# Optimization experiments

Hardware: AMD Instinct MI355X
Metric: run time of the kernel (lower is better)

## Reference

```python
import jax, jax.numpy as jnp
import numpy as np

N = 40000        # nodes (shared across categories)
E = 600000       # edges per category graph
H = 2            # heads
C = 64           # hidden (out_channels per head)
IN_DIMS = [128, 128, 64]
FUSED = H * C * len(IN_DIMS)  # 384


def setup_inputs() -> dict:
    key = jax.random.key(0)
    ks = iter(jax.random.split(key, 64))
    d = {}
    for i, din in enumerate(IN_DIMS):
        d[f"x{i}"] = jax.random.normal(next(ks), (N, din), jnp.float32)
        d[f"ei{i}"] = jax.random.randint(next(ks), (2, E), 0, N)
        d[f"W{i}"] = jax.random.normal(next(ks), (din, H * C), jnp.float32) / np.sqrt(din)
        d[f"att_s{i}"] = jax.random.normal(next(ks), (H, C), jnp.float32) * 0.1
        d[f"att_d{i}"] = jax.random.normal(next(ks), (H, C), jnp.float32) * 0.1
        d[f"bias{i}"] = jnp.zeros((H * C,), jnp.float32)
    d["Wc1"] = jax.random.normal(next(ks), (FUSED, 128), jnp.float32) / np.sqrt(FUSED)
    d["bc1"] = jnp.zeros((128,), jnp.float32)
    d["Wc2"] = jax.random.normal(next(ks), (128, 1), jnp.float32) / np.sqrt(128.0)
    d["bc2"] = jnp.zeros((1,), jnp.float32)
    return d


def gat_conv(x, edge_index, W, att_s, att_d, bias):
    """PyG GATConv (concat=True, add_self_loops=True, eval mode)."""
    n = x.shape[0]
    xw = (x @ W).reshape(n, H, C)                       # [N,H,C]
    a_src = jnp.einsum('nhc,hc->nh', xw, att_s)         # [N,H]
    a_dst = jnp.einsum('nhc,hc->nh', xw, att_d)         # [N,H]
    loop = jnp.arange(n)
    src = jnp.concatenate([edge_index[0], loop])        # [E+N]
    dst = jnp.concatenate([edge_index[1], loop])
    e = jax.nn.leaky_relu(a_src[src] + a_dst[dst], 0.2)  # [E+N,H]
    # segment softmax over incoming edges per destination node
    m = jax.lax.stop_gradient(jax.ops.segment_max(e, dst, num_segments=n))
    ex = jnp.exp(e - m[dst])
    s = jax.ops.segment_sum(ex, dst, num_segments=n)
    alpha = ex / s[dst]                                  # [E+N,H]
    out = jax.ops.segment_sum(xw[src] * alpha[..., None], dst, num_segments=n)
    return out.reshape(n, H * C) + bias


def reference(x0, ei0, W0, att_s0, att_d0, bias0,
              x1, ei1, W1, att_s1, att_d1, bias1,
              x2, ei2, W2, att_s2, att_d2, bias2,
              Wc1, bc1, Wc2, bc2):
    h0 = jax.nn.elu(gat_conv(x0, ei0, W0, att_s0, att_d0, bias0))
    h1 = jax.nn.elu(gat_conv(x1, ei1, W1, att_s1, att_d1, bias1))
    h2 = jax.nn.elu(gat_conv(x2, ei2, W2, att_s2, att_d2, bias2))
    Hcat = jnp.concatenate([h0, h1, h2], axis=-1)        # [N, FUSED]
    hid = jax.nn.relu(Hcat @ Wc1 + bc1)
    return hid @ Wc2 + bc2                               # [N, 1]
```

## Files before the change

### kernel.cpp

```cpp
#include <hip/hip_runtime.h>
#include <hip/hip_fp16.h>
#include <cstdint>
#include <cstddef>


__device__ __forceinline__ float lrelu02(float x) { return x > 0.f ? x : 0.2f * x; }
__device__ __forceinline__ float elu1(float x) { return x > 0.f ? x : (__expf(x) - 1.f); }

__device__ __forceinline__ unsigned bfrne(float x) {
  unsigned u = __float_as_uint(x);
  return (u + 0x7FFFu + ((u >> 16) & 1u)) >> 16;
}
__device__ __forceinline__ unsigned pack2bf(float lo, float hi) {
  return bfrne(lo) | (bfrne(hi) << 16);
}
__device__ __forceinline__ float bflo2f(unsigned u) { return __uint_as_float(u << 16); }
__device__ __forceinline__ float bfhi2f(unsigned u) { return __uint_as_float(u & 0xFFFF0000u); }

__device__ __forceinline__ unsigned pack2half(float lo, float hi) {
  __half2 h2 = __floats2half2_rn(lo, hi);
  return __builtin_bit_cast(unsigned, h2);
}
__device__ __forceinline__ float h2lo(unsigned u) {
  return __half2float(__low2half(__builtin_bit_cast(__half2, u)));
}
__device__ __forceinline__ float h2hi(unsigned u) {
  return __half2float(__high2half(__builtin_bit_cast(__half2, u)));
}

typedef __attribute__((ext_vector_type(8))) short short8;
typedef __attribute__((ext_vector_type(4))) float f32x4;

#define SLICES 8
#define CAPX 448
#define BCAP (SLICES * CAPX)

#define SBS 512
#define SEPT 16
#define STB (SBS * SEPT)
#define NBINS_PAD 1024

__global__ void zeroB(int* __restrict__ a, int n) {
  int i = blockIdx.x * blockDim.x + threadIdx.x;
  if (i < n) a[i] = 0;
}

__global__ void w_swz(const float* __restrict__ W,
                      unsigned short* __restrict__ wsw, int nt) {
  int idx = blockIdx.x * blockDim.x + threadIdx.x;
  if (idx >= nt * 8 * 64) return;
  int l = idx & 63;
  int n = (idx >> 6) & 7;
  int t = idx >> 9;
  int col = n * 16 + (l & 15);
  int kbase = t * 32 + (l >> 4) * 8;
  uint4 o;
  o.x = pack2bf(W[(kbase + 0) * 128 + col], W[(kbase + 1) * 128 + col]);
  o.y = pack2bf(W[(kbase + 2) * 128 + col], W[(kbase + 3) * 128 + col]);
  o.z = pack2bf(W[(kbase + 4) * 128 + col], W[(kbase + 5) * 128 + col]);
  o.w = pack2bf(W[(kbase + 6) * 128 + col], W[(kbase + 7) * 128 + col]);
  *(uint4*)(wsw + (size_t)idx * 8) = o;
}

__global__ __launch_bounds__(256) void gemm_att_mfma(
    const float* __restrict__ X, const unsigned short* __restrict__ wsw,
    const float* __restrict__ att_s, const float* __restrict__ att_d,
    unsigned short* __restrict__ XWH, float* __restrict__ a_src,
    float* __restrict__ a_dst, int M, int K) {
  const int tid = threadIdx.x;
  const int l = tid & 63;
  const int w = tid >> 6;
  const int lrow = l & 15;
  const int lk = (l >> 4) * 8;
  const int row0 = blockIdx.x * 64 + w * 16;
  int arow = row0 + lrow; if (arow >= M) arow = M - 1;
  const float* aptr = X + (size_t)arow * K + lk;
  const unsigned short* bptr = wsw + (size_t)l * 8;
  const int nt = K >> 5;

  f32x4 acc[8];
#pragma unroll
  for (int n = 0; n < 8; ++n) acc[n] = (f32x4){0.f, 0.f, 0.f, 0.f};

  for (int t = 0; t < nt; ++t) {
    float4 xa = *(const float4*)(aptr + t * 32);
    float4 xb = *(const float4*)(aptr + t * 32 + 4);
    uint4 av;
    av.x = pack2bf(xa.x, xa.y);
    av.y = pack2bf(xa.z, xa.w);
    av.z = pack2bf(xb.x, xb.y);
    av.w = pack2bf(xb.z, xb.w);
    short8 af = __builtin_bit_cast(short8, av);
#pragma unroll
    for (int n = 0; n < 8; ++n) {
      uint4 bv = *(const uint4*)(bptr + (size_t)(t * 8 + n) * 512);
      short8 bf = __builtin_bit_cast(short8, bv);
      acc[n] = __builtin_amdgcn_mfma_f32_16x16x32_bf16(af, bf, acc[n], 0, 0, 0);
    }
  }

  float as_[8], ad_[8];
#pragma unroll
  for (int n = 0; n < 8; ++n) {
    int col = n * 16 + lrow;
    as_[n] = att_s[col];
    ad_[n] = att_d[col];
  }
#pragma unroll
  for (int r = 0; r < 4; ++r) {
    int wrow = row0 + (l >> 4) * 4 + r;
    const bool ok = wrow < M;
    float ps0 = 0.f, ps1 = 0.f, pd0 = 0.f, pd1 = 0.f;
#pragma unroll
    for (int n = 0; n < 8; ++n) {
      float v = acc[n][r];
      if (ok) XWH[(size_t)wrow * 128 + n * 16 + lrow] = (unsigned short)bfrne(v);
      if (n < 4) { ps0 = fmaf(v, as_[n], ps0); pd0 = fmaf(v, ad_[n], pd0); }
      else       { ps1 = fmaf(v, as_[n], ps1); pd1 = fmaf(v, ad_[n], pd1); }
    }
#pragma unroll
    for (int off = 1; off < 16; off <<= 1) {
      ps0 += __shfl_xor(ps0, off); ps1 += __shfl_xor(ps1, off);
      pd0 += __shfl_xor(pd0, off); pd1 += __shfl_xor(pd1, off);
    }
    if (lrow == 0 && ok) {
      ((float2*)a_src)[wrow] = make_float2(ps0, ps1);
      ((float2*)a_dst)[wrow] = make_float2(pd0, pd1);
    }
  }
}

__global__ __launch_bounds__(512) void scatter_p(
    const int* __restrict__ ei0, const int* __restrict__ ei1,
    const int* __restrict__ ei2, int E0, int E1, int E2,
    int nbpc, int* __restrict__ bktCnt, int* __restrict__ bkt) {
  __shared__ int hist[NBINS_PAD];
  __shared__ int binStart[NBINS_PAD];
  __shared__ int binResv[NBINS_PAD];
  __shared__ int fillB[NBINS_PAD];
  __shared__ int scanBuf[SBS];
  __shared__ int stage[STB];
  __shared__ int gdst[STB];
  const int tid = threadIdx.x;
  const int slice = blockIdx.x & (SLICES - 1);
  const int nbins = 3 * nbpc;
  const int c1 = E0, c2 = E0 + E1, totE = c2 + E2;
  const int eb = blockIdx.x * STB;

  for (int b = tid; b < NBINS_PAD; b += SBS) hist[b] = 0;
  __syncthreads();

  int binv[SEPT], payv[SEPT];
#pragma unroll
  for (int k = 0; k < SEPT; ++k) {
    int g = eb + k * SBS + tid;
    int bn = -1, pay = 0;
    if (g < totE) {
      int s, d, cat;
      if (g < c1)      { s = ei0[g]; d = ei0[E0 + g]; cat = 0; }
      else if (g < c2) { int t = g - c1; s = ei1[t]; d = ei1[E1 + t]; cat = 1; }
      else             { int t = g - c2; s = ei2[t]; d = ei2[E2 + t]; cat = 2; }
      bn = cat * nbpc + (d >> 7);
      pay = ((d & 127) << 16) | s;
      atomicAdd(&hist[bn], 1);
    }
    binv[k] = bn; payv[k] = pay;
  }
  __syncthreads();

  const int a0 = hist[tid * 2], a1 = hist[tid * 2 + 1];
  scanBuf[tid] = a0 + a1;
  __syncthreads();
  for (int off = 1; off < SBS; off <<= 1) {
    int v = (tid >= off) ? scanBuf[tid - off] : 0;
    __syncthreads();
    scanBuf[tid] += v;
    __syncthreads();
  }
  const int total = scanBuf[SBS - 1];
  const int base = (tid > 0) ? scanBuf[tid - 1] : 0;
  binStart[tid * 2] = base;
  binStart[tid * 2 + 1] = base + a0;

  for (int b = tid; b < NBINS_PAD; b += SBS) {
    fillB[b] = 0;
    int c = hist[b];
    if (c > 0 && b < nbins)
      binResv[b] = atomicAdd(&bktCnt[(b * SLICES + slice) * 16], c);
  }
  __syncthreads();

#pragma unroll
  for (int k = 0; k < SEPT; ++k) {
    int bn = binv[k];
    if (bn >= 0) {
      int f = atomicAdd(&fillB[bn], 1);
      int p = binStart[bn] + f;
      int go = binResv[bn] + f;
      stage[p] = payv[k];
      gdst[p] = (go < CAPX) ? ((bn * SLICES + slice) * CAPX + go) : -1;
    }
  }
  __syncthreads();

  for (int i = tid; i < total; i += SBS) {
    int g = gdst[i];
    if (g >= 0) bkt[g] = stage[i];
  }
}

__global__ __launch_bounds__(256) void sortbkt(
    int* __restrict__ bkt, const int* __restrict__ bktCnt,
    int2* __restrict__ offcnt, int Nn, int nbpc) {
  __shared__ int cntA[128], scanA[128], fillA[128];
  __shared__ int esort[BCAP];
  const int tid = threadIdx.x;
  const int b = blockIdx.x;
  const int cat = b / nbpc, bl = b - cat * nbpc, dBase = bl << 7;
  if (tid < 128) {
    cntA[tid] = (dBase + tid < Nn) ? 1 : 0;
    fillA[tid] = 0;
  }
  __syncthreads();
  int ns[SLICES];
#pragma unroll
  for (int s = 0; s < SLICES; ++s)
    ns[s] = min(bktCnt[(b * SLICES + s) * 16], CAPX);
#pragma unroll
  for (int s = 0; s < SLICES; ++s) {
    const int* seg = bkt + (size_t)(b * SLICES + s) * CAPX;
    for (int i = tid; i < ns[s]; i += 256) atomicAdd(&cntA[seg[i] >> 16], 1);
  }
  __syncthreads();
  if (tid < 128) scanA[tid] = cntA[tid];
  __syncthreads();
  for (int off = 1; off < 128; off <<= 1) {
    int t = (tid < 128 && tid >= off) ? scanA[tid - off] : 0;
    __syncthreads();
    if (tid < 128) scanA[tid] += t;
    __syncthreads();
  }
#pragma unroll
  for (int s = 0; s < SLICES; ++s) {
    const int* seg = bkt + (size_t)(b * SLICES + s) * CAPX;
    for (int i = tid; i < ns[s]; i += 256) {
      int v = seg[i];
      int n = v >> 16;
      int p = scanA[n] - cntA[n] + atomicAdd(&fillA[n], 1);
      esort[p] = v & 0xFFFF;
    }
  }
  if (tid < 128 && dBase + tid < Nn) esort[scanA[tid] - 1] = dBase + tid;
  __syncthreads();
  const int tot = scanA[127];
  int* outp = bkt + (size_t)b * BCAP;
  for (int i = tid; i < tot; i += 256) outp[i] = esort[i];
  if (tid < 128 && dBase + tid < Nn)
    offcnt[(size_t)cat * Nn + dBase + tid] =
        make_int2(b * BCAP + scanA[tid] - cntA[tid], cntA[tid]);
}

__global__ __launch_bounds__(256) void aggregate(
    const unsigned short* __restrict__ xwh, const float* __restrict__ a_src,
    const float* __restrict__ a_dst, const int2* __restrict__ offcnt,
    const int* __restrict__ adjS, const float* __restrict__ bias,
    unsigned short* __restrict__ ahc, int Nn) {
  const int tid = threadIdx.x;
  const int lane = tid & 63;
  const int li = lane & 15;
  const int gb = lane & 48;
  const int wid = (int)((blockIdx.x * (size_t)blockDim.x + tid) >> 6);
  const int node = wid * 4 + (lane >> 4);
  const bool nok = node < Nn;
  const int cnode = nok ? node : Nn - 1;
  const int2 oc = offcnt[cnode];
  const int base = oc.x;
  const int cnt = oc.y;
  const float2 ad = ((const float2*)a_dst)[cnode];

  float m0 = -1e30f, s0 = 0.f, m1 = -1e30f, s1 = 0.f;
  int sv0 = 0; float ex0 = -1e30f, ey0 = -1e30f;
  for (int cb = 0; cb < cnt; cb += 16) {
    int sv = 0; float ex = -1e30f, ey = -1e30f;
    if (cb + li < cnt) {
      sv = adjS[base + cb + li];
      float2 as = ((const float2*)a_src)[sv];
      ex = lrelu02(as.x + ad.x);
      ey = lrelu02(as.y + ad.y);
      float nm0 = fmaxf(m0, ex);
      s0 = s0 * __expf(m0 - nm0) + __expf(ex - nm0); m0 = nm0;
      float nm1 = fmaxf(m1, ey);
      s1 = s1 * __expf(m1 - nm1) + __expf(ey - nm1); m1 = nm1;
    }
    if (cb == 0) { sv0 = sv; ex0 = ex; ey0 = ey; }
  }
#pragma unroll
  for (int off = 8; off; off >>= 1) {
    float om0 = __shfl_xor(m0, off), os0 = __shfl_xor(s0, off);
    float nm0 = fmaxf(m0, om0);
    s0 = s0 * __expf(m0 - nm0) + os0 * __expf(om0 - nm0); m0 = nm0;
    float om1 = __shfl_xor(m1, off), os1 = __shfl_xor(s1, off);
    float nm1 = fmaxf(m1, om1);
    s1 = s1 * __expf(m1 - nm1) + os1 * __expf(om1 - nm1); m1 = nm1;
  }
  const float inv0 = 1.f / s0, inv1 = 1.f / s1;

  int mc = cnt;
  mc = max(mc, __shfl_xor(mc, 16));
  mc = max(mc, __shfl_xor(mc, 32));

  const bool hlo = (li < 8);
  float acc[8];
#pragma unroll
  for (int c = 0; c < 8; ++c) acc[c] = 0.f;

  for (int cb = 0; cb < mc; cb += 16) {
    int sv; float ex, ey;
    if (cb == 0) { sv = sv0; ex = ex0; ey = ey0; }
    else {
      sv = 0; ex = -1e30f; ey = -1e30f;
      if (cb + li < cnt) {
        sv = adjS[base + cb + li];
        float2 as = ((const float2*)a_src)[sv];
        ex = lrelu02(as.x + ad.x);
        ey = lrelu02(as.y + ad.y);
      }
    }
    const float w0 = __expf(ex - m0) * inv0;
    const float w1 = __expf(ey - m1) * inv1;
    const unsigned wpk = pack2half(w0, w1);

    int cc = cnt - cb; cc = cc < 0 ? 0 : (cc > 16 ? 16 : cc);
    cc = max(cc, __shfl_xor(cc, 16));
    cc = max(cc, __shfl_xor(cc, 32));

    int k = 0;
    for (; k + 2 <= cc; k += 2) {
      int ska = __shfl(sv, gb + k);
      int skb = __shfl(sv, gb + k + 1);
      unsigned wka = __shfl(wpk, gb + k);
      unsigned wkb = __shfl(wpk, gb + k + 1);
      uint4 ua = *(const uint4*)(xwh + (size_t)ska * 128 + li * 8);
      uint4 ub = *(const uint4*)(xwh + (size_t)skb * 128 + li * 8);
      float wa = hlo ? h2lo(wka) : h2hi(wka);
      float wb = hlo ? h2lo(wkb) : h2hi(wkb);
      acc[0] = fmaf(wa, bflo2f(ua.x), acc[0]); acc[1] = fmaf(wa, bfhi2f(ua.x), acc[1]);
      acc[2] = fmaf(wa, bflo2f(ua.y), acc[2]); acc[3] = fmaf(wa, bfhi2f(ua.y), acc[3]);
      acc[4] = fmaf(wa, bflo2f(ua.z), acc[4]); acc[5] = fmaf(wa, bfhi2f(ua.z), acc[5]);
      acc[6] = fmaf(wa, bflo2f(ua.w), acc[6]); acc[7] = fmaf(wa, bfhi2f(ua.w), acc[7]);
      acc[0] = fmaf(wb, bflo2f(ub.x), acc[0]); acc[1] = fmaf(wb, bfhi2f(ub.x), acc[1]);
      acc[2] = fmaf(wb, bflo2f(ub.y), acc[2]); acc[3] = fmaf(wb, bfhi2f(ub.y), acc[3]);
      acc[4] = fmaf(wb, bflo2f(ub.z), acc[4]); acc[5] = fmaf(wb, bfhi2f(ub.z), acc[5]);
      acc[6] = fmaf(wb, bflo2f(ub.w), acc[6]); acc[7] = fmaf(wb, bfhi2f(ub.w), acc[7]);
    }
    for (; k < cc; ++k) {
      int sk = __shfl(sv, gb + k);
      unsigned wk = __shfl(wpk, gb + k);
      float w = hlo ? h2lo(wk) : h2hi(wk);
      uint4 u = *(const uint4*)(xwh + (size_t)sk * 128 + li * 8);
      acc[0] = fmaf(w, bflo2f(u.x), acc[0]); acc[1] = fmaf(w, bfhi2f(u.x), acc[1]);
      acc[2] = fmaf(w, bflo2f(u.y), acc[2]); acc[3] = fmaf(w, bfhi2f(u.y), acc[3]);
      acc[4] = fmaf(w, bflo2f(u.z), acc[4]); acc[5] = fmaf(w, bfhi2f(u.z), acc[5]);
      acc[6] = fmaf(w, bflo2f(u.w), acc[6]); acc[7] = fmaf(w, bfhi2f(u.w), acc[7]);
    }
  }

  if (nok) {
    const float4 b0 = *(const float4*)(bias + li * 8);
    const float4 b1 = *(const float4*)(bias + li * 8 + 4);
    uint4 o;
    o.x = pack2bf(elu1(acc[0] + b0.x), elu1(acc[1] + b0.y));
    o.y = pack2bf(elu1(acc[2] + b0.z), elu1(acc[3] + b0.w));
    o.z = pack2bf(elu1(acc[4] + b1.x), elu1(acc[5] + b1.y));
    o.w = pack2bf(elu1(acc[6] + b1.z), elu1(acc[7] + b1.w));
    *(uint4*)(ahc + (size_t)node * 384 + li * 8) = o;
  }
}

__global__ __launch_bounds__(256) void final_mlp_mfma(
    const unsigned short* __restrict__ ah, const unsigned short* __restrict__ wsw,
    const float* __restrict__ bc1, const float* __restrict__ Wc2,
    const float* __restrict__ bc2, float* __restrict__ out, int Nn) {
  const int tid = threadIdx.x;
  const int l = tid & 63;
  const int w = tid >> 6;
  const int lrow = l & 15;
  const int lk = (l >> 4) * 8;
  int row = blockIdx.x * 64 + w * 16 + lrow;
  int arow = row < Nn ? row : Nn - 1;
  const unsigned short* aptr = ah + (size_t)arow * 384 + lk;
  const unsigned short* bptr = wsw + (size_t)l * 8;

  f32x4 acc[8];
#pragma unroll
  for (int n = 0; n < 8; ++n) acc[n] = (f32x4){0.f, 0.f, 0.f, 0.f};

  for (int t = 0; t < 12; ++t) {
    uint4 av = *(const uint4*)(aptr + t * 32);
    short8 af = __builtin_bit_cast(short8, av);
#pragma unroll
    for (int n = 0; n < 8; ++n) {
      uint4 bv = *(const uint4*)(bptr + (size_t)(t * 8 + n) * 512);
      short8 bf = __builtin_bit_cast(short8, bv);
      acc[n] = __builtin_amdgcn_mfma_f32_16x16x32_bf16(af, bf, acc[n], 0, 0, 0);
    }
  }

  float bcv[8], w2v[8];
#pragma unroll
  for (int n = 0; n < 8; ++n) {
    int col = n * 16 + lrow;
    bcv[n] = bc1[col];
    w2v[n] = Wc2[col];
  }
  float p[4];
#pragma unroll
  for (int r = 0; r < 4; ++r) {
    float s = 0.f;
#pragma unroll
    for (int n = 0; n < 8; ++n)
      s = fmaf(fmaxf(acc[n][r] + bcv[n], 0.f), w2v[n], s);
#pragma unroll
    for (int off = 1; off < 16; off <<= 1) s += __shfl_xor(s, off);
    p[r] = s;
  }
  if (lrow == 0) {
    int orow = blockIdx.x * 64 + w * 16 + (l >> 4) * 4;
    float b2 = bc2[0];
    if (orow + 3 < Nn) {
      float4 o = {p[0] + b2, p[1] + b2, p[2] + b2, p[3] + b2};
      *(float4*)(out + orow) = o;
    } else {
#pragma unroll
      for (int r = 0; r < 4; ++r)
        if (orow + r < Nn) out[orow + r] = p[r] + b2;
    }
  }
}

extern "C" void kernel_launch(void* const* d_in, const int* in_sizes, int n_in,
                              void* d_out, int out_size, void* d_ws, size_t ws_size,
                              hipStream_t stream) {
  const int Nn = out_size;
  const int E0 = in_sizes[1] / 2;
  const int E1 = in_sizes[7] / 2;
  const int E2 = in_sizes[13] / 2;
  const int totE = E0 + E1 + E2;
  const int Nt = 3 * Nn;
  const int nbpc = (Nn + 127) / 128;
  const int NB = 3 * nbpc;

  char* base = (char*)d_ws;
  size_t off = 0;
  auto carve = [&](size_t bytes) -> void* {
    off = (off + 255) & ~(size_t)255;
    void* p = base + off;
    off += bytes;
    return p;
  };
  unsigned short* xwh = (unsigned short*)carve((size_t)Nn * 128 * 2);
  unsigned short* ah  = (unsigned short*)carve((size_t)Nn * 384 * 2);
  unsigned short* wsw = (unsigned short*)carve((size_t)12 * 8 * 64 * 8 * 2);
  unsigned short* wswx = (unsigned short*)carve((size_t)3 * 4 * 8 * 64 * 8 * 2);
  float* a_src3 = (float*)carve((size_t)Nt * 2 * 4);
  float* a_dst3 = (float*)carve((size_t)Nt * 2 * 4);
  int*  bktCnt  = (int*)carve((size_t)NB * SLICES * 16 * 4);
  int2* offcnt3 = (int2*)carve((size_t)Nt * 8);
  int*  bkt     = (int*)carve((size_t)NB * BCAP * 4);
  (void)ws_size; (void)n_in;

  const int* ei0 = (const int*)d_in[1];
  const int* ei1 = (const int*)d_in[7];
  const int* ei2 = (const int*)d_in[13];

  const int ncnt = NB * SLICES * 16;
  zeroB<<<(ncnt + 255) / 256, 256, 0, stream>>>(bktCnt, ncnt);
  w_swz<<<(12 * 8 * 64 + 255) / 256, 256, 0, stream>>>(
      (const float*)d_in[18], wsw, 12);
  for (int cat = 0; cat < 3; ++cat) {
    const int K = in_sizes[6 * cat] / Nn;
    w_swz<<<((K >> 5) * 8 * 64 + 255) / 256, 256, 0, stream>>>(
        (const float*)d_in[6 * cat + 2], wswx + (size_t)cat * 4 * 8 * 64 * 8,
        K >> 5);
  }
  scatter_p<<<(totE + STB - 1) / STB, SBS, 0, stream>>>(
      ei0, ei1, ei2, E0, E1, E2, nbpc, bktCnt, bkt);
  sortbkt<<<NB, 256, 0, stream>>>(bkt, bktCnt, offcnt3, Nn, nbpc);

  for (int cat = 0; cat < 3; ++cat) {
    const float* x   = (const float*)d_in[6 * cat + 0];
    const float* ats = (const float*)d_in[6 * cat + 3];
    const float* atd = (const float*)d_in[6 * cat + 4];
    const float* bia = (const float*)d_in[6 * cat + 5];
    const int K = in_sizes[6 * cat] / Nn;
    float* a_src_c = a_src3 + (size_t)cat * Nn * 2;
    float* a_dst_c = a_dst3 + (size_t)cat * Nn * 2;

    gemm_att_mfma<<<(Nn + 63) / 64, 256, 0, stream>>>(
        x, wswx + (size_t)cat * 4 * 8 * 64 * 8, ats, atd, xwh,
        a_src_c, a_dst_c, Nn, K);
    aggregate<<<(Nn + 15) / 16, 256, 0, stream>>>(
        xwh, a_src_c, a_dst_c, offcnt3 + (size_t)cat * Nn, bkt, bia,
        ah + (size_t)cat * 128, Nn);
  }

  final_mlp_mfma<<<(Nn + 63) / 64, 256, 0, stream>>>(
      ah, wsw, (const float*)d_in[19], (const float*)d_in[20],
      (const float*)d_in[21], (float*)d_out, Nn);
}
```

Before: 296.6 us.

## Batch three categories into single GEMM/aggregate launches with degree-sorted node order

Merges the per-category GEMM and aggregation launches into one grid each, using blockIdx.y or a global index to select the category, with a separate XWH buffer per category. Adds a counting sort of nodes by in-degree (histogram, scan, place) so each wavefront handles four nodes of similar degree, cutting divergence and idle lanes in the aggregate loop. This removes launch overhead and serialization between categories and raises occupancy. In exchange it adds three small kernels with atomics, an indirection through perm, and a scattered write order into the output.

```diff
diff --git a/kernel.cpp b/kernel.cpp
--- a/kernel.cpp
+++ b/kernel.cpp
@@ -39,6 +39,7 @@
 #define SEPT 16
 #define STB (SBS * SEPT)
 #define NBINS_PAD 1024
+#define DBINS 1024
 
 __global__ void zeroB(int* __restrict__ a, int n) {
   int i = blockIdx.x * blockDim.x + threadIdx.x;
@@ -63,10 +64,22 @@
 }
 
 __global__ __launch_bounds__(256) void gemm_att_mfma(
-    const float* __restrict__ X, const unsigned short* __restrict__ wsw,
-    const float* __restrict__ att_s, const float* __restrict__ att_d,
-    unsigned short* __restrict__ XWH, float* __restrict__ a_src,
-    float* __restrict__ a_dst, int M, int K) {
+    const float* __restrict__ X0, const float* __restrict__ X1,
+    const float* __restrict__ X2, const unsigned short* __restrict__ wswx,
+    const float* __restrict__ as0, const float* __restrict__ as1,
+    const float* __restrict__ as2, const float* __restrict__ ad0,
+    const float* __restrict__ ad1, const float* __restrict__ ad2,
+    unsigned short* __restrict__ XWH3, float* __restrict__ a_src3,
+    float* __restrict__ a_dst3, int M, int K0, int K1, int K2) {
+  const int cat = blockIdx.y;
+  const float* X = (cat == 0) ? X0 : (cat == 1) ? X1 : X2;
+  const float* att_s = (cat == 0) ? as0 : (cat == 1) ? as1 : as2;
+  const float* att_d = (cat == 0) ? ad0 : (cat == 1) ? ad1 : ad2;
+  const int K = (cat == 0) ? K0 : (cat == 1) ? K1 : K2;
+  unsigned short* XWH = XWH3 + (size_t)cat * M * 128;
+  float* a_src = a_src3 + (size_t)cat * M * 2;
+  float* a_dst = a_dst3 + (size_t)cat * M * 2;
+
   const int tid = threadIdx.x;
   const int l = tid & 63;
   const int w = tid >> 6;
@@ -75,7 +88,7 @@
   const int row0 = blockIdx.x * 64 + w * 16;
   int arow = row0 + lrow; if (arow >= M) arow = M - 1;
   const float* aptr = X + (size_t)arow * K + lk;
-  const unsigned short* bptr = wsw + (size_t)l * 8;
+  const unsigned short* bptr = wswx + (size_t)cat * (4 * 8 * 64 * 8) + (size_t)l * 8;
   const int nt = K >> 5;
 
   f32x4 acc[8];
@@ -260,23 +273,68 @@
         make_int2(b * BCAP + scanA[tid] - cntA[tid], cntA[tid]);
 }
 
+__global__ void dhist(const int2* __restrict__ offcnt3, int* __restrict__ db,
+                      int Nn) {
+  int i = blockIdx.x * blockDim.x + threadIdx.x;
+  if (i >= 3 * Nn) return;
+  int cat = i / Nn;
+  int bin = min(offcnt3[i].y, DBINS - 1);
+  atomicAdd(&db[cat * DBINS + bin], 1);
+}
+__global__ void dscan(int* __restrict__ db) {
+  __shared__ int psum[256];
+  int* d = db + blockIdx.x * DBINS;
+  const int t = threadIdx.x;
+  int loc[DBINS / 256];
+  int s = 0;
+#pragma unroll
+  for (int j = 0; j < DBINS / 256; ++j) { loc[j] = d[t * (DBINS / 256) + j]; s += loc[j]; }
+  psum[t] = s;
+  __syncthreads();
+  for (int off = 1; off < 256; off <<= 1) {
+    int v = (t >= off) ? psum[t - off] : 0;
+    __syncthreads();
+    psum[t] += v;
+    __syncthreads();
+  }
+  int ex = (t > 0) ? psum[t - 1] : 0;
+#pragma unroll
+  for (int j = 0; j < DBINS / 256; ++j) { int c = loc[j]; d[t * (DBINS / 256) + j] = ex; ex += c; }
+}
+__global__ void dplace(const int2* __restrict__ offcnt3, int* __restrict__ db,
+                       int* __restrict__ perm, int Nn) {
+  int i = blockIdx.x * blockDim.x + threadIdx.x;
+  if (i >= 3 * Nn) return;
+  int cat = i / Nn, node = i - cat * Nn;
+  int bin = min(offcnt3[i].y, DBINS - 1);
+  int r = atomicAdd(&db[cat * DBINS + bin], 1);
+  perm[cat * Nn + r] = node;
+}
+
 __global__ __launch_bounds__(256) void aggregate(
-    const unsigned short* __restrict__ xwh, const float* __restrict__ a_src,
-    const float* __restrict__ a_dst, const int2* __restrict__ offcnt,
-    const int* __restrict__ adjS, const float* __restrict__ bias,
-    unsigned short* __restrict__ ahc, int Nn) {
+    const unsigned short* __restrict__ xwh3, const float* __restrict__ a_src3,
+    const float* __restrict__ a_dst3, const int2* __restrict__ offcnt3,
+    const int* __restrict__ adjS, const int* __restrict__ perm,
+    const float* __restrict__ b0p, const float* __restrict__ b1p,
+    const float* __restrict__ b2p, unsigned short* __restrict__ ahc, int Nn) {
   const int tid = threadIdx.x;
   const int lane = tid & 63;
   const int li = lane & 15;
   const int gb = lane & 48;
   const int wid = (int)((blockIdx.x * (size_t)blockDim.x + tid) >> 6);
-  const int node = wid * 4 + (lane >> 4);
-  const bool nok = node < Nn;
-  const int cnode = nok ? node : Nn - 1;
-  const int2 oc = offcnt[cnode];
+  int gidx = wid * 4 + (lane >> 4);
+  const bool nok = gidx < 3 * Nn;
+  if (!nok) gidx = 3 * Nn - 1;
+  const int cat = gidx / Nn;
+  const int lnode = perm[gidx];
+  const int ci = cat * Nn + lnode;
+  const int2 oc = offcnt3[ci];
   const int base = oc.x;
   const int cnt = oc.y;
-  const float2 ad = ((const float2*)a_dst)[cnode];
+  const float2 ad = ((const float2*)a_dst3)[ci];
+  const float2* asrc = (const float2*)a_src3 + (size_t)cat * Nn;
+  const unsigned short* xwh = xwh3 + (size_t)cat * Nn * 128;
+  const float* bias = (cat == 0) ? b0p : (cat == 1) ? b1p : b2p;
 
   float m0 = -1e30f, s0 = 0.f, m1 = -1e30f, s1 = 0.f;
   int sv0 = 0; float ex0 = -1e30f, ey0 = -1e30f;
@@ -284,7 +342,7 @@
     int sv = 0; float ex = -1e30f, ey = -1e30f;
     if (cb + li < cnt) {
       sv = adjS[base + cb + li];
-      float2 as = ((const float2*)a_src)[sv];
+      float2 as = asrc[sv];
       ex = lrelu02(as.x + ad.x);
       ey = lrelu02(as.y + ad.y);
       float nm0 = fmaxf(m0, ex);
@@ -321,7 +379,7 @@
       sv = 0; ex = -1e30f; ey = -1e30f;
       if (cb + li < cnt) {
         sv = adjS[base + cb + li];
-        float2 as = ((const float2*)a_src)[sv];
+        float2 as = asrc[sv];
         ex = lrelu02(as.x + ad.x);
         ey = lrelu02(as.y + ad.y);
       }
@@ -373,7 +431,7 @@
     o.y = pack2bf(elu1(acc[2] + b0.z), elu1(acc[3] + b0.w));
     o.z = pack2bf(elu1(acc[4] + b1.x), elu1(acc[5] + b1.y));
     o.w = pack2bf(elu1(acc[6] + b1.z), elu1(acc[7] + b1.w));
-    *(uint4*)(ahc + (size_t)node * 384 + li * 8) = o;
+    *(uint4*)(ahc + (size_t)lnode * 384 + cat * 128 + li * 8) = o;
   }
 }
 
@@ -458,15 +516,17 @@
     off += bytes;
     return p;
   };
-  unsigned short* xwh = (unsigned short*)carve((size_t)Nn * 128 * 2);
-  unsigned short* ah  = (unsigned short*)carve((size_t)Nn * 384 * 2);
-  unsigned short* wsw = (unsigned short*)carve((size_t)12 * 8 * 64 * 8 * 2);
+  unsigned short* xwh3 = (unsigned short*)carve((size_t)Nt * 128 * 2);
+  unsigned short* ah   = (unsigned short*)carve((size_t)Nn * 384 * 2);
+  unsigned short* wsw  = (unsigned short*)carve((size_t)12 * 8 * 64 * 8 * 2);
   unsigned short* wswx = (unsigned short*)carve((size_t)3 * 4 * 8 * 64 * 8 * 2);
   float* a_src3 = (float*)carve((size_t)Nt * 2 * 4);
   float* a_dst3 = (float*)carve((size_t)Nt * 2 * 4);
   int*  bktCnt  = (int*)carve((size_t)NB * SLICES * 16 * 4);
   int2* offcnt3 = (int2*)carve((size_t)Nt * 8);
   int*  bkt     = (int*)carve((size_t)NB * BCAP * 4);
+  int*  db      = (int*)carve((size_t)3 * DBINS * 4);
+  int*  perm    = (int*)carve((size_t)Nt * 4);
   (void)ws_size; (void)n_in;
 
   const int* ei0 = (const int*)d_in[1];
@@ -475,6 +535,7 @@
 
   const int ncnt = NB * SLICES * 16;
   zeroB<<<(ncnt + 255) / 256, 256, 0, stream>>>(bktCnt, ncnt);
+  zeroB<<<(3 * DBINS + 255) / 256, 256, 0, stream>>>(db, 3 * DBINS);
   w_swz<<<(12 * 8 * 64 + 255) / 256, 256, 0, stream>>>(
       (const float*)d_in[18], wsw, 12);
   for (int cat = 0; cat < 3; ++cat) {
@@ -486,23 +547,23 @@
   scatter_p<<<(totE + STB - 1) / STB, SBS, 0, stream>>>(
       ei0, ei1, ei2, E0, E1, E2, nbpc, bktCnt, bkt);
   sortbkt<<<NB, 256, 0, stream>>>(bkt, bktCnt, offcnt3, Nn, nbpc);
-
-  for (int cat = 0; cat < 3; ++cat) {
-    const float* x   = (const float*)d_in[6 * cat + 0];
-    const float* ats = (const float*)d_in[6 * cat + 3];
-    const float* atd = (const float*)d_in[6 * cat + 4];
-    const float* bia = (const float*)d_in[6 * cat + 5];
-    const int K = in_sizes[6 * cat] / Nn;
-    float* a_src_c = a_src3 + (size_t)cat * Nn * 2;
-    float* a_dst_c = a_dst3 + (size_t)cat * Nn * 2;
-
-    gemm_att_mfma<<<(Nn + 63) / 64, 256, 0, stream>>>(
-        x, wswx + (size_t)cat * 4 * 8 * 64 * 8, ats, atd, xwh,
-        a_src_c, a_dst_c, Nn, K);
-    aggregate<<<(Nn + 15) / 16, 256, 0, stream>>>(
-        xwh, a_src_c, a_dst_c, offcnt3 + (size_t)cat * Nn, bkt, bia,
-        ah + (size_t)cat * 128, Nn);
-  }
+  dhist<<<(Nt + 255) / 256, 256, 0, stream>>>(offcnt3, db, Nn);
+  dscan<<<3, 256, 0, stream>>>(db);
+  dplace<<<(Nt + 255) / 256, 256, 0, stream>>>(offcnt3, db, perm, Nn);
+
+  dim3 gg((Nn + 63) / 64, 3);
+  gemm_att_mfma<<<gg, 256, 0, stream>>>(
+      (const float*)d_in[0], (const float*)d_in[6], (const float*)d_in[12],
+      wswx,
+      (const float*)d_in[3], (const float*)d_in[9], (const float*)d_in[15],
+      (const float*)d_in[4], (const float*)d_in[10], (const float*)d_in[16],
+      xwh3, a_src3, a_dst3, Nn,
+      in_sizes[0] / Nn, in_sizes[6] / Nn, in_sizes[12] / Nn);
+
+  aggregate<<<(Nt + 15) / 16, 256, 0, stream>>>(
+      xwh3, a_src3, a_dst3, offcnt3, bkt, perm,
+      (const float*)d_in[5], (const float*)d_in[11], (const float*)d_in[17],
+      ah, Nn);
 
   final_mlp_mfma<<<(Nn + 63) / 64, 256, 0, stream>>>(
       ah, wsw, (const float*)d_in[19], (const float*)d_in[20],
```

Result: slower. 557.3 us (+87.9%).
